# Kernel optimization log

Measured on AMD Instinct MI355X. Metric: run time of the kernel, lower is better.

Reference implementation:

```python
import jax, jax.numpy as jnp
import numpy as np

# dims: batch, history P, horizon Q, hidden D, nodes N, cells C=H*W, Z channels
B_, P_, Q_, D_, N_, C_, H_, W_, CZ = 16, 12, 12, 64, 2000, 1024, 32, 32, 2
K_DIFF = 3  # max diffusion step of DCGRUCell -> K+1 Chebyshev terms


def _mlp2(x, w1, b1, w2, b2):
    return jax.nn.relu(x @ w1 + b1) @ w2 + b2


def _st_embedding(SE, TE, sw1, sb1, sw2, sb2, tw1, tb1, tw2, tb2):
    # GMAN-style spatio-temporal embedding: SE (M,D), TE (B,P,2) ints
    se = _mlp2(SE, sw1, sb1, sw2, sb2)                                  # (M, D)
    te = jnp.concatenate([jax.nn.one_hot(TE[..., 0], 7, dtype=SE.dtype),
                          jax.nn.one_hot(TE[..., 1], 288, dtype=SE.dtype)], axis=-1)
    te = _mlp2(te, tw1, tb1, tw2, tb2)                                  # (B, P, D)
    return se[None, None] + te[:, :, None, :]                           # (B, P, M, D)


def _scaled_laplacian(adj):
    # DCRNN 'laplacian' filter: L_tilde = 2 L / lambda_max - I, lambda_max ~= 2
    A = jnp.maximum(adj, adj.T)
    d = A.sum(axis=1)
    dinv = jnp.where(d > 0, jax.lax.rsqrt(d), 0.0)
    eye = jnp.eye(A.shape[0], dtype=A.dtype)
    L = eye - (dinv[:, None] * A) * dinv[None, :]
    return L - eye


def _gconv(x, L, K):
    # Chebyshev diffusion features: x (B,N,F) -> (B,N,F*(K+1))
    xs = [x, jnp.einsum('nm,bmf->bnf', L, x)]
    for _ in range(2, K + 1):
        xs.append(2.0 * jnp.einsum('nm,bmf->bnf', L, xs[-1]) - xs[-2])
    b, n, f = x.shape
    return jnp.stack(xs, axis=-1).reshape(b, n, f * (K + 1))


def _hard_sigmoid(x):
    return jnp.clip(0.2 * x + 0.5, 0.0, 1.0)


def _conv2d(x, w):
    return jax.lax.conv_general_dilated(x, w, (1, 1), 'SAME',
        dimension_numbers=('NHWC', 'HWIO', 'NHWC'))


def _forward(X, Z, TE, adj_gg, adj_gr, gumbel_noise, se_x, se_z, movement_logits,
             stex_se_w1, stex_se_b1, stex_se_w2, stex_se_b2,
             stex_te_w1, stex_te_b1, stex_te_w2, stex_te_b2,
             stez_se_w1, stez_se_b1, stez_se_w2, stez_se_b2,
             stez_te_w1, stez_te_b1, stez_te_w2, stez_te_b2,
             fcs_z_w1, fcs_z_b1, fcs_z_w2, fcs_z_b2,
             fcs_x_in_w1, fcs_x_in_b1, fcs_x_in_w2, fcs_x_in_b2,
             mov_fc_w, mov_fc_b,
             fcs_x_out_w1, fcs_x_out_b1, fcs_x_out_w2, fcs_x_out_b2,
             convlstm_wx, convlstm_wh,
             dcgru_gate_w, dcgru_gate_b, dcgru_cand_w, dcgru_cand_b):
    B = X.shape[0]
    TEp = TE.astype(jnp.int32)[:, :P_, :]
    # --- cell branch ---
    STEZ = _st_embedding(se_z, TEp, stez_se_w1, stez_se_b1, stez_se_w2, stez_se_b2,
                         stez_te_w1, stez_te_b1, stez_te_w2, stez_te_b2)
    Zf = _mlp2(Z, fcs_z_w1, fcs_z_b1, fcs_z_w2, fcs_z_b2) + STEZ          # (B,P,C,D)
    Zg = Zf.reshape(B, P_, H_, W_, D_)
    def clstm_step(carry, x):
        h, c = carry
        gates = _conv2d(x, convlstm_wx) + _conv2d(h, convlstm_wh)         # (B,H,W,4D)
        i, f, g, o = jnp.split(gates, 4, axis=-1)
        c = _hard_sigmoid(f) * c + _hard_sigmoid(i) * jnp.tanh(g)
        h = _hard_sigmoid(o) * jnp.tanh(c)
        return (h, c), h
    hc0 = (jnp.zeros((B, H_, W_, D_), X.dtype), jnp.zeros((B, H_, W_, D_), X.dtype))
    _, hs = jax.lax.scan(clstm_step, hc0, jnp.swapaxes(Zg, 0, 1))
    Zc = jnp.swapaxes(hs, 0, 1).reshape(B, P_, C_, D_)
    # gumbel-softmax routing over cells (soft, tau=1)
    g = -jnp.log(-jnp.log(gumbel_noise + 1e-20) + 1e-20)
    mZ = jax.nn.softmax(movement_logits + g, axis=-1)                     # (C,C)
    Zc = jnp.einsum('cd,bpdk->bpck', mZ, Zc)
    Zc = jax.nn.relu(Zc @ mov_fc_w + mov_fc_b)
    ZX = jnp.einsum('nc,bpck->bpnk', adj_gr, Zc)                          # (B,P,N,D)
    # --- node branch ---
    STEX = _st_embedding(se_x, TEp, stex_se_w1, stex_se_b1, stex_se_w2, stex_se_b2,
                         stex_te_w1, stex_te_b1, stex_te_w2, stex_te_b2)
    Xf = _mlp2(X[..., None], fcs_x_in_w1, fcs_x_in_b1, fcs_x_in_w2, fcs_x_in_b2) + STEX + ZX
    L = _scaled_laplacian(adj_gg)
    def dcgru_step(h, x):
        xh = jnp.concatenate([x, h], axis=-1)                             # (B,N,2D)
        ru = jax.nn.sigmoid(_gconv(xh, L, K_DIFF) @ dcgru_gate_w + dcgru_gate_b)
        r, u = jnp.split(ru, 2, axis=-1)
        cnd = jnp.tanh(_gconv(jnp.concatenate([x, r * h], axis=-1), L, K_DIFF)
                       @ dcgru_cand_w + dcgru_cand_b)
        return u * h + (1.0 - u) * cnd, None
    h_last, _ = jax.lax.scan(dcgru_step, jnp.zeros((B, N_, D_), X.dtype),
                             jnp.swapaxes(Xf, 0, 1))                      # (B,N,D)
    Y = _mlp2(h_last, fcs_x_out_w1, fcs_x_out_b1, fcs_x_out_w2, fcs_x_out_b2)  # (B,N,Q)
    return jnp.transpose(Y, (0, 2, 1))                                    # (B,Q,N)


def setup_inputs() -> dict:
    key = jax.random.key(0)
    ks = iter(jax.random.split(key, 64))
    def rn(shape, s=0.05):
        return jax.random.normal(next(ks), shape, dtype=jnp.float32) * s
    def ru(shape):
        return jax.random.uniform(next(ks), shape, dtype=jnp.float32)
    z = lambda *s: jnp.zeros(s, jnp.float32)
    NM = K_DIFF + 1
    inp = {
        'X': rn((B_, P_, N_), 1.0),
        'Z': rn((B_, P_, C_, CZ), 1.0),
        'TE': jax.random.randint(next(ks), (B_, P_ + Q_, 2), 0, 7, dtype=jnp.int32),
        'adj_gg': ru((N_, N_)),
        'adj_gr': ru((N_, C_)) * 0.01,
        'gumbel_noise': jnp.clip(ru((C_, C_)), 1e-6, 1.0 - 1e-6),
        'se_x': rn((N_, D_)), 'se_z': rn((C_, D_)),
        'movement_logits': rn((C_, C_)),
        'stex_se_w1': rn((D_, D_)), 'stex_se_b1': z(D_), 'stex_se_w2': rn((D_, D_)), 'stex_se_b2': z(D_),
        'stex_te_w1': rn((295, D_)), 'stex_te_b1': z(D_), 'stex_te_w2': rn((D_, D_)), 'stex_te_b2': z(D_),
        'stez_se_w1': rn((D_, D_)), 'stez_se_b1': z(D_), 'stez_se_w2': rn((D_, D_)), 'stez_se_b2': z(D_),
        'stez_te_w1': rn((295, D_)), 'stez_te_b1': z(D_), 'stez_te_w2': rn((D_, D_)), 'stez_te_b2': z(D_),
        'fcs_z_w1': rn((CZ, D_)), 'fcs_z_b1': z(D_), 'fcs_z_w2': rn((D_, D_)), 'fcs_z_b2': z(D_),
        'fcs_x_in_w1': rn((1, D_)), 'fcs_x_in_b1': z(D_), 'fcs_x_in_w2': rn((D_, D_)), 'fcs_x_in_b2': z(D_),
        'mov_fc_w': rn((D_, D_)), 'mov_fc_b': z(D_),
        'fcs_x_out_w1': rn((D_, D_)), 'fcs_x_out_b1': z(D_), 'fcs_x_out_w2': rn((D_, Q_)), 'fcs_x_out_b2': z(Q_),
        'convlstm_wx': rn((3, 3, D_, 4 * D_)), 'convlstm_wh': rn((3, 3, D_, 4 * D_)),
        'dcgru_gate_w': rn((2 * D_ * NM, 2 * D_)), 'dcgru_gate_b': z(2 * D_),
        'dcgru_cand_w': rn((2 * D_ * NM, D_)), 'dcgru_cand_b': z(D_),
    }
    return inp


def reference(X, Z, TE, adj_gg, adj_gr, gumbel_noise, se_x, se_z, movement_logits,
              stex_se_w1, stex_se_b1, stex_se_w2, stex_se_b2,
              stex_te_w1, stex_te_b1, stex_te_w2, stex_te_b2,
              stez_se_w1, stez_se_b1, stez_se_w2, stez_se_b2,
              stez_te_w1, stez_te_b1, stez_te_w2, stez_te_b2,
              fcs_z_w1, fcs_z_b1, fcs_z_w2, fcs_z_b2,
              fcs_x_in_w1, fcs_x_in_b1, fcs_x_in_w2, fcs_x_in_b2,
              mov_fc_w, mov_fc_b,
              fcs_x_out_w1, fcs_x_out_b1, fcs_x_out_w2, fcs_x_out_b2,
              convlstm_wx, convlstm_wh,
              dcgru_gate_w, dcgru_gate_b, dcgru_cand_w, dcgru_cand_b):
    return _forward(X, Z, TE, adj_gg, adj_gr, gumbel_noise, se_x, se_z, movement_logits,
                    stex_se_w1, stex_se_b1, stex_se_w2, stex_se_b2,
                    stex_te_w1, stex_te_b1, stex_te_w2, stex_te_b2,
                    stez_se_w1, stez_se_b1, stez_se_w2, stez_se_b2,
                    stez_te_w1, stez_te_b1, stez_te_w2, stez_te_b2,
                    fcs_z_w1, fcs_z_b1, fcs_z_w2, fcs_z_b2,
                    fcs_x_in_w1, fcs_x_in_b1, fcs_x_in_w2, fcs_x_in_b2,
                    mov_fc_w, mov_fc_b,
                    fcs_x_out_w1, fcs_x_out_b1, fcs_x_out_w2, fcs_x_out_b2,
                    convlstm_wx, convlstm_wh,
                    dcgru_gate_w, dcgru_gate_b, dcgru_cand_w, dcgru_cand_b)
```

## Files before the change

kernel.cpp:

```cpp
#include <hip/hip_runtime.h>
#include <hip/hip_bf16.h>
#include <math.h>

typedef _Float16 fp16;
typedef _Float16 f16x8 __attribute__((ext_vector_type(8)));
typedef float f32x4 __attribute__((ext_vector_type(4)));

#define BB 16
#define PP 12
#define QQ 12
#define NN 2000
#define CC 1024
#define GP 34
#define GP2 1156

static __device__ __forceinline__ float ldf(float v) { return v; }
static __device__ __forceinline__ float ldf(fp16 v) { return (float)v; }
static __device__ __forceinline__ void stf(float* p, float v) { *p = v; }
static __device__ __forceinline__ void stf(fp16* p, float v) { *p = (fp16)v; }

static __device__ __forceinline__ void gload_lds16(const fp16* g, fp16* l) {
  __builtin_amdgcn_global_load_lds(
      (const __attribute__((address_space(1))) void*)g,
      (__attribute__((address_space(3))) void*)l, 16, 0, 0);
}


__global__ void k_f2h(fp16* __restrict__ dst, const float* __restrict__ src, long long n) {
  long long i = (long long)blockIdx.x * 256 + threadIdx.x;
  if (i < n) dst[i] = (fp16)src[i];
}

__global__ void k_wcatT(fp16* __restrict__ dst, const float* __restrict__ w39,
                        const float* __restrict__ w40) {
  int i = blockIdx.x * 256 + threadIdx.x;
  if (i >= 1152 * 256) return;
  int n = i & 255, kk = i >> 8;
  float v = (kk < 576) ? w39[kk * 256 + n] : w40[(kk - 576) * 256 + n];
  dst[(long long)n * 1152 + kk] = (fp16)v;
}

__global__ void k_gru_repackT(fp16* __restrict__ dst, const float* __restrict__ src, int O) {
  int i = blockIdx.x * 256 + threadIdx.x;
  if (i >= O * 512) return;
  int d = i >> 9;
  int kc = i & 511;
  int t = kc >> 7;
  int c = kc & 127;
  dst[i] = (fp16)src[(c * 4 + t) * O + d];
}

__global__ void k_w2T(fp16* __restrict__ dst, const float* __restrict__ src) {
  int i = blockIdx.x * 256 + threadIdx.x;
  if (i >= 4096) return;
  int d = i >> 6, k = i & 63;
  dst[i] = (fp16)src[k * 64 + d];
}

__global__ void k_wT(fp16* __restrict__ dst, const float* __restrict__ src, int J, int JP) {
  int i = blockIdx.x * 256 + threadIdx.x;
  if (i >= JP * 64) return;
  int j = i >> 6, k = i & 63;
  dst[i] = (fp16)((j < J) ? src[k * J + j] : 0.f);
}

__global__ void k_dinv(const float* __restrict__ adj, float* __restrict__ dinv) {
  int row = blockIdx.x;
  float s = 0.f;
  for (int j = threadIdx.x; j < NN; j += 256)
    s += fmaxf(adj[(long long)row * NN + j], adj[(long long)j * NN + row]);
  __shared__ float red[256];
  red[threadIdx.x] = s;
// ... 11 lines not shown
__global__ void k_L(const float* __restrict__ adj, const float* __restrict__ dinv,
                    fp16* __restrict__ Lh) {
  long long i = (long long)blockIdx.x * 256 + threadIdx.x;
  if (i >= (long long)NN * NN) return;
  int r = (int)(i / NN), c = (int)(i % NN);
  float a = fmaxf(adj[(long long)r * NN + c], adj[(long long)c * NN + r]);
  Lh[(long long)r * 2048 + c] = (fp16)(-dinv[r] * a * dinv[c]);
}

__global__ void k_subdiag(fp16* __restrict__ M2) {
  int i = blockIdx.x * 256 + threadIdx.x;
  if (i >= NN) return;
  M2[(long long)i * 2048 + i] = (fp16)((float)M2[(long long)i * 2048 + i] - 1.0f);
}

__global__ void k_gumbel_softmax(const float* __restrict__ ml, const float* __restrict__ gn,
                                 fp16* __restrict__ mZ) {
  int row = blockIdx.x;
  __shared__ float buf[CC];
  __shared__ float red[256];
  int t = threadIdx.x;
  float mx = -1e30f;
  for (int j = t; j < CC; j += 256) {
    float u = gn[(long long)row * CC + j];
    float g = -logf(-logf(u + 1e-20f) + 1e-20f);
    float v = ml[(long long)row * CC + j] + g;
    buf[j] = v;
    mx = fmaxf(mx, v);
  }
  red[t] = mx;
  __syncthreads();
  for (int st = 128; st > 0; st >>= 1) {
    if (t < st) red[t] = fmaxf(red[t], red[t + st]);
    __syncthreads();
  }
  mx = red[0];
  __syncthreads();
  float s = 0.f;
  for (int j = t; j < CC; j += 256) {
    float e = expf(buf[j] - mx);
    buf[j] = e;
    s += e;
  }
  red[t] = s;
  __syncthreads();
  for (int st = 128; st > 0; st >>= 1) {
    if (t < st) red[t] += red[t + st];
    __syncthreads();
  }
  float inv = 1.0f / red[0];
  for (int j = t; j < CC; j += 256) mZ[(long long)row * CC + j] = (fp16)(buf[j] * inv);
}

__global__ void k_te(const int* __restrict__ TE, const float* __restrict__ w1,
                     const float* __restrict__ b1, float* __restrict__ tmp) {
  int i = blockIdx.x * 256 + threadIdx.x;
  if (i >= BB * PP * 64) return;
  int j = i & 63;
  int bp = i >> 6;
  int b = bp / PP, p = bp % PP;
  int te0 = TE[(b * (PP + QQ) + p) * 2 + 0];
  int te1 = TE[(b * (PP + QQ) + p) * 2 + 1];
  float v = w1[te0 * 64 + j] + w1[(7 + te1) * 64 + j] + b1[j];
  tmp[i] = fmaxf(v, 0.f);
}

__global__ void k_addb(float* __restrict__ dst, const float* __restrict__ b, int n) {
  int i = blockIdx.x * 256 + threadIdx.x;
  if (i < n) dst[i] += b[i & 63];
}

__global__ __launch_bounds__(256) void k_zf2f(
    const float* __restrict__ Z, const float* __restrict__ w25,
    const float* __restrict__ b26, const fp16* __restrict__ w27T,
    const float* __restrict__ b28, const float* __restrict__ seZ,
    const float* __restrict__ teZ, fp16* __restrict__ Zfp) {
  __shared__ fp16 As[128 * 64];
  __shared__ fp16 Bs[64 * 64];
  const int tid = threadIdx.x;
  const int gm0 = blockIdx.x * 128;
  const int lane = tid & 63, wv = tid >> 6;
  const int wr = wv >> 1, wc = wv & 1;
  const int quad = lane >> 4, ln = lane & 15;
#pragma unroll
  for (int i = 0; i < 4; ++i) {
    int c = i * 256 + tid;
    int row = c >> 3, seg = c & 7;
    float z0v = Z[(long long)(gm0 + row) * 2 + 0];
    float z1v = Z[(long long)(gm0 + row) * 2 + 1];
    fp16 tmp[8];
#pragma unroll
    for (int e = 0; e < 8; ++e) {
      int j = seg * 8 + e;
      tmp[e] = (fp16)fmaxf(z0v * w25[j] + z1v * w25[64 + j] + b26[j], 0.f);
    }
    *(f16x8*)&As[row * 64 + ((seg ^ (row & 7)) * 8)] = *(f16x8*)tmp;
  }
#pragma unroll
  for (int i = 0; i < 2; ++i) {
    int c = i * 256 + tid;
    int row = c >> 3;
    int lseg = (c & 7) ^ (row & 7);
    gload_lds16(w27T + (long long)row * 64 + lseg * 8, &Bs[c * 8]);
  }
  f32x4 acc[4][2];
#pragma unroll
  for (int i = 0; i < 4; ++i)
#pragma unroll
    for (int j = 0; j < 2; ++j) acc[i][j] = (f32x4){0.f, 0.f, 0.f, 0.f};
  __syncthreads();
#pragma unroll
  for (int kt = 0; kt < 2; ++kt) {
    f16x8 af[4], bf[2];
#pragma unroll
    for (int wm = 0; wm < 4; ++wm) {
      int row = wr * 64 + wm * 16 + ln;
      int slot = (kt * 4 + quad) ^ (row & 7);
      af[wm] = *(const f16x8*)&As[row * 64 + slot * 8];
    }
#pragma unroll
    for (int wn = 0; wn < 2; ++wn) {
      int row = wc * 32 + wn * 16 + ln;
// ... 63 lines not shown
    f16x8 af[4], bf[2];
#pragma unroll
    for (int wm = 0; wm < 4; ++wm) {
      int row = wr * 64 + wm * 16 + ln;
      af[wm] = *(const f16x8*)&hT[row * 72 + kt * 32 + quad * 8];
    }
#pragma unroll
    for (int wn = 0; wn < 2; ++wn) {
      int row = wc * 32 + wn * 16 + ln;
      int slot = (kt * 4 + quad) ^ (row & 7);
      bf[wn] = *(const f16x8*)&Bs[row * 64 + slot * 8];
    }
#pragma unroll
    for (int wm = 0; wm < 4; ++wm)
#pragma unroll
      for (int wn = 0; wn < 2; ++wn)
        a1[wm][wn] =
            __builtin_amdgcn_mfma_f32_16x16x32_f16(af[wm], bf[wn], a1[wm][wn], 0, 0, 0);
  }
#pragma unroll
  for (int wm = 0; wm < 4; ++wm)
#pragma unroll
    for (int wn = 0; wn < 2; ++wn)
#pragma unroll
      for (int r = 0; r < 4; ++r) {
        int rl = wr * 64 + wm * 16 + quad * 4 + r;
        int j = wc * 32 + wn * 16 + ln;
        h2[rl * 72 + j] = (fp16)fmaxf(a1[wm][wn][r] + b36[j], 0.f);
      }
  __syncthreads();
  f32x4 a2[2];
#pragma unroll
  for (int i = 0; i < 2; ++i) a2[i] = (f32x4){0.f, 0.f, 0.f, 0.f};
#pragma unroll
  for (int kt = 0; kt < 2; ++kt) {
    f16x8 bf = *(const f16x8*)(w37T + ln * 64 + kt * 32 + quad * 8);
#pragma unroll
    for (int wm = 0; wm < 2; ++wm) {
      int row = wv * 32 + wm * 16 + ln;
      f16x8 af = *(const f16x8*)&h2[row * 72 + kt * 32 + quad * 8];
      a2[wm] = __builtin_amdgcn_mfma_f32_16x16x32_f16(af, bf, a2[wm], 0, 0, 0);
    }
  }
#pragma unroll
  for (int wm = 0; wm < 2; ++wm)
#pragma unroll
    for (int r = 0; r < 4; ++r) {
      int nl = wv * 32 + wm * 16 + quad * 4 + r;
      int n = n0 + nl;
      int q = ln;
      if (n < NN && q < 12)
        out[((long long)b * 12 + q) * NN + n] = a2[wm][r] + b38[q];
    }
}

template <typename TA, typename TB, typename TC>
__global__ __launch_bounds__(256) void gemm_t(
    const TA* __restrict__ A, int lda, long long sA,
    const TB* __restrict__ Bm, int ldb, long long sB,
    TC* Cm, int ldc, long long sC,
    const TC* S, long long sS,
    const float* __restrict__ bias,
    int M, int Ncols, int K, float alpha, float beta, int act) {
  int bz = blockIdx.z;
  A += (long long)bz * sA;
  Bm += (long long)bz * sB;
  Cm += (long long)bz * sC;
  if (S) S += (long long)bz * sS;
  const int row0 = blockIdx.x * 64, col0 = blockIdx.y * 64;
  __shared__ float As[16][68];
  __shared__ float Bs[16][68];
  int tid = threadIdx.x, tx = tid & 15, ty = tid >> 4;
  float acc[4][4] = {};
  for (int k0 = 0; k0 < K; k0 += 16) {
#pragma unroll
    for (int j = 0; j < 4; ++j) {
      int e = tid + 256 * j;
      int m = e >> 4, kk = e & 15;
      int gm = row0 + m;
      As[kk][m] = (gm < M) ? ldf(A[(long long)gm * lda + k0 + kk]) : 0.f;
    }
#pragma unroll
    for (int j = 0; j < 4; ++j) {
      int e = tid + 256 * j;
      int kk = e >> 6, n = e & 63;
      int gn = col0 + n;
      Bs[kk][n] = (gn < Ncols) ? ldf(Bm[(long long)(k0 + kk) * ldb + gn]) : 0.f;
    }
    __syncthreads();
#pragma unroll
    for (int kk = 0; kk < 16; ++kk) {
      float a[4], bb[4];
#pragma unroll
      for (int i = 0; i < 4; ++i) a[i] = As[kk][ty * 4 + i];
#pragma unroll
      for (int j = 0; j < 4; ++j) bb[j] = Bs[kk][tx * 4 + j];
#pragma unroll
      for (int i = 0; i < 4; ++i)
#pragma unroll
        for (int j = 0; j < 4; ++j) acc[i][j] = fmaf(a[i], bb[j], acc[i][j]);
    }
    __syncthreads();
  }
#pragma unroll
  for (int i = 0; i < 4; ++i) {
    int r = row0 + ty * 4 + i;
    if (r >= M) continue;
#pragma unroll
    for (int j = 0; j < 4; ++j) {
      int cn = col0 + tx * 4 + j;
      if (cn >= Ncols) continue;
      float v = alpha * acc[i][j];
      if (bias) v += bias[cn];
      if (S) v += beta * ldf(S[(long long)r * ldc + cn]);
      if (act == 1) v = fmaxf(v, 0.f);
      else if (act == 2) v = 1.f / (1.f + expf(-v));
      else if (act == 3) v = tanhf(v);
      stf(&Cm[(long long)r * ldc + cn], v);
    }
  }
}

template <int MT, int MODE>
__global__ __launch_bounds__(256) void mfma7(
    const fp16* __restrict__ A,
    const fp16* __restrict__ U0base, long long uZ, int bHi,
    const fp16* __restrict__ xB, long long xZ,
    const fp16* __restrict__ Xc, long long XcSlab, int Xcld, int Xczmul,
    const fp16* __restrict__ Hc, long long HcSlab, int Hcld, int Hczmul,
    fp16* __restrict__ C, int ldc, long long cBatch,
    const float* __restrict__ bias,
    fp16* __restrict__ rhOut, const fp16* __restrict__ hIn,
    const fp16* __restrict__ uIn, long long uStride,
    int M, int Ncols) {
  __shared__ fp16 As[2][MT * 32];
  __shared__ fp16 Bs[2][64 * 32];
  const int z = blockIdx.z;
  const int n0 = blockIdx.y * 64;
  const fp16* U0z = U0base + (long long)z * uZ;
  const fp16* xBz = xB + (long long)z * xZ;
  C += (long long)z * cBatch;
  if (rhOut) rhOut += (long long)z * uZ;
  if (hIn) hIn += (long long)z * uZ;
  if (uIn) uIn += (long long)z * uStride;
  const int tid = threadIdx.x;
  const int lane = tid & 63, wv = tid >> 6;
  const int wr = wv >> 1, wc = wv & 1;
  const int quad = lane >> 4, ln = lane & 15;
  constexpr int WM = MT / 32;

  const fp16* aSrc[MT / 64];
#pragma unroll
  for (int i = 0; i < MT / 64; ++i) {
    int c = i * 256 + tid;
    int row = c >> 2;
    int lseg = (c & 3) ^ ((c >> 3) & 3);
    aSrc[i] = A + (long long)row * 512 + lseg * 8;
  }
  const int brow = tid >> 2;
  const int blseg = (tid & 3) ^ ((tid >> 3) & 3);
  const long long bnode = n0 + brow;

  f32x4 acc[WM][2];
#pragma unroll
  for (int i = 0; i < WM; ++i)
#pragma unroll
    for (int j = 0; j < 2; ++j) acc[i][j] = (f32x4){0.f, 0.f, 0.f, 0.f};

  auto stage = [&](int t, int buf) {
    const int k0 = t * 32;
#pragma unroll
    for (int i = 0; i < MT / 64; ++i)
      gload_lds16(aSrc[i] + k0, &As[buf][(i * 256 + tid) * 8]);
// ... 337 lines not shown

  const int sw = (quad ^ ((ln >> 1) & 3)) << 3;

#pragma unroll
  for (int i = 0; i < MT / 64; ++i) gload_lds16(aSrc[i], &As[0][(i * 256 + tid) * 8]);
#pragma unroll
  for (int i = 0; i < NT / 64; ++i) gload_lds16(bSrc[i], &Bs[0][(i * 256 + tid) * 8]);

  const int nk = K >> 5;
  for (int t = 0; t < nk; ++t) {
    const int buf = t & 1;
    __syncthreads();
    if (t + 1 < nk) {
      const int k1 = (t + 1) * 32;
#pragma unroll
      for (int i = 0; i < MT / 64; ++i)
        gload_lds16(aSrc[i] + k1, &As[buf ^ 1][(i * 256 + tid) * 8]);
#pragma unroll
      for (int i = 0; i < NT / 64; ++i)
        gload_lds16(bSrc[i] + k1, &Bs[buf ^ 1][(i * 256 + tid) * 8]);
    }
    f16x8 af[WM], bf[WN];
#pragma unroll
    for (int wm = 0; wm < WM; ++wm) {
      int row = wr * (MT / 2) + wm * 16 + ln;
      af[wm] = *(const f16x8*)&As[buf][row * 32 + sw];
    }
#pragma unroll
    for (int wn = 0; wn < WN; ++wn) {
      int row = wc * (NT / 2) + wn * 16 + ln;
      bf[wn] = *(const f16x8*)&Bs[buf][row * 32 + sw];
    }
#pragma unroll
    for (int wm = 0; wm < WM; ++wm)
#pragma unroll
      for (int wn = 0; wn < WN; ++wn)
        acc[wm][wn] =
            __builtin_amdgcn_mfma_f32_16x16x32_f16(af[wm], bf[wn], acc[wm][wn], 0, 0, 0);
  }
#pragma unroll
  for (int wm = 0; wm < WM; ++wm)
#pragma unroll
    for (int wn = 0; wn < WN; ++wn)
#pragma unroll
      for (int r = 0; r < 4; ++r) {
        int gm = gm0 + wr * (MT / 2) + wm * 16 + quad * 4 + r;
        int gn = n0 + wc * (NT / 2) + wn * 16 + ln;
        long long ci = ((long long)((unsigned)gm >> cMsh)) * cMslab +
                       (long long)(gm & cMmask) * ldc + gn;
        C[ci] = (fp16)acc[wm][wn][r];
      }
}

__global__ __launch_bounds__(256) void k_zxtfin2(
    const fp16* __restrict__ w2T, const float* __restrict__ X,
    const float* __restrict__ w29, const float* __restrict__ b30,
    fp16* __restrict__ ZXt, const float* __restrict__ teXb,
    const float* __restrict__ seX) {
  __shared__ fp16 As[64][72];
  __shared__ fp16 Bs[128][72];
  const int z = blockIdx.z;
  const int n0 = blockIdx.y * 128;
  fp16* Cz = ZXt + (long long)z * 64 * 2048;
  const float* tb = teXb + z * 64;
  const int tid = threadIdx.x;
  const int lane = tid & 63, wv = tid >> 6;
  const int wr = wv >> 1, wc = wv & 1;
  const int quad = lane >> 4, ln = lane & 15;
#pragma unroll
  for (int i = 0; i < 2; ++i) {
    int c = tid + 256 * i;
    int row = c >> 3, seg = c & 7;
    *(f16x8*)&As[row][seg * 8] = *(const f16x8*)(w2T + row * 64 + seg * 8);
  }
#pragma unroll
  for (int i = 0; i < 4; ++i) {
    int c = tid + 256 * i;
    int row = c >> 3, seg = c & 7;
    int n = n0 + row;
    float xv = (n < NN) ? X[(long long)z * NN + n] : 0.f;
    fp16 tmp[8];
#pragma unroll
    for (int e = 0; e < 8; ++e) {
      int j = seg * 8 + e;
      tmp[e] = (fp16)fmaxf(xv * w29[j] + b30[j], 0.f);
    }
    *(f16x8*)&Bs[row][seg * 8] = *(f16x8*)tmp;
  }
  __syncthreads();
  f32x4 acc[2][4];
#pragma unroll
  for (int i = 0; i < 2; ++i)
#pragma unroll
    for (int j = 0; j < 4; ++j) acc[i][j] = (f32x4){0.f, 0.f, 0.f, 0.f};
#pragma unroll
  for (int kt = 0; kt < 2; ++kt) {
    f16x8 af[2], bf[4];
#pragma unroll
    for (int wm = 0; wm < 2; ++wm)
      af[wm] = *(const f16x8*)&As[wr * 32 + wm * 16 + ln][kt * 32 + quad * 8];
#pragma unroll
    for (int wn = 0; wn < 4; ++wn)
      bf[wn] = *(const f16x8*)&Bs[wc * 64 + wn * 16 + ln][kt * 32 + quad * 8];
#pragma unroll
    for (int wm = 0; wm < 2; ++wm)
#pragma unroll
      for (int wn = 0; wn < 4; ++wn)
        acc[wm][wn] =
            __builtin_amdgcn_mfma_f32_16x16x32_f16(af[wm], bf[wn], acc[wm][wn], 0, 0, 0);
  }
#pragma unroll
  for (int wm = 0; wm < 2; ++wm)
#pragma unroll
    for (int wn = 0; wn < 4; ++wn)
#pragma unroll
      for (int r = 0; r < 4; ++r) {
        int gm = wr * 32 + wm * 16 + quad * 4 + r;
        int gn = n0 + wc * 64 + wn * 16 + ln;
        long long ci = (long long)gm * 2048 + gn;
        float v = 0.f;
        if (gn < NN)
          v = acc[wm][wn][r] + (float)Cz[ci] + tb[gm] + seX[(long long)gn * 64 + gm];
        Cz[ci] = (fp16)v;
      }
}

__global__ __launch_bounds__(256) void k_conv4(
    const fp16* __restrict__ Zfp, const fp16* __restrict__ hp,
    const fp16* __restrict__ wcatT, fp16* __restrict__ gates, int p) {
  __shared__ fp16 As[2][128 * 32];
  __shared__ fp16 Bs[2][64 * 32];
  const int gm0 = blockIdx.x * 128, n0 = blockIdx.y * 64;
  const int tid = threadIdx.x;
  const int lane = tid & 63, wv = tid >> 6;
  const int wr = wv >> 1, wc = wv & 1;
  const int quad = lane >> 4, ln = lane & 15;

  long long aZ[2], aH[2];
#pragma unroll
  for (int i = 0; i < 2; ++i) {
    int c = tid + 256 * i;
    int row = c >> 2;
    int lseg = (c & 3) ^ ((c >> 3) & 3);
    int m = gm0 + row;
    int b = m >> 10, y = (m >> 5) & 31, x = m & 31;
    int pc = (y + 1) * GP + (x + 1);
    aZ[i] = ((long long)(b * PP + p) * GP2 + pc) * 64 + lseg * 8;
    aH[i] = ((long long)b * GP2 + pc) * 64 + lseg * 8;
  }
  const fp16* bBase;
  {
    int row = tid >> 2;
    int lseg = (tid & 3) ^ ((tid >> 3) & 3);
    bBase = wcatT + (long long)(n0 + row) * 1152 + lseg * 8;
  }
  f32x4 acc[4][2];
#pragma unroll
  for (int i = 0; i < 4; ++i)
#pragma unroll
    for (int j = 0; j < 2; ++j) acc[i][j] = (f32x4){0.f, 0.f, 0.f, 0.f};

  auto stage = [&](int t, int buf) {
    int tap = (t >> 1) % 9, half = t & 1;
    int srcsel = t >= 18;
    int off = ((tap / 3 - 1) * GP + (tap % 3 - 1)) * 64 + half * 32;
#pragma unroll
    for (int i = 0; i < 2; ++i) {
      const fp16* src = srcsel ? (hp + aH[i] + off) : (Zfp + aZ[i] + off);
      gload_lds16(src, &As[buf][(i * 256 + tid) * 8]);
    }
    gload_lds16(bBase + t * 32, &Bs[buf][tid * 8]);
  };
  stage(0, 0);
  const int sw = (quad ^ ((ln >> 1) & 3)) << 3;
  for (int t = 0; t < 36; ++t) {
    const int buf = t & 1;
// ... 1 lines not shown
    if (t + 1 < 36) stage(t + 1, buf ^ 1);
    f16x8 af[4], bf[2];
#pragma unroll
    for (int wm = 0; wm < 4; ++wm) {
      int row = wr * 64 + wm * 16 + ln;
      af[wm] = *(const f16x8*)&As[buf][row * 32 + sw];
    }
#pragma unroll
    for (int wn = 0; wn < 2; ++wn) {
      int row = wc * 32 + wn * 16 + ln;
      bf[wn] = *(const f16x8*)&Bs[buf][row * 32 + sw];
    }
#pragma unroll
    for (int wm = 0; wm < 4; ++wm)
#pragma unroll
      for (int wn = 0; wn < 2; ++wn)
        acc[wm][wn] =
            __builtin_amdgcn_mfma_f32_16x16x32_f16(af[wm], bf[wn], acc[wm][wn], 0, 0, 0);
  }
#pragma unroll
  for (int wm = 0; wm < 4; ++wm)
#pragma unroll
    for (int wn = 0; wn < 2; ++wn)
#pragma unroll
      for (int r = 0; r < 4; ++r) {
        int gm = gm0 + wr * 64 + wm * 16 + quad * 4 + r;
        int gn = n0 + wc * 32 + wn * 16 + ln;
        gates[(long long)gm * 256 + gn] = (fp16)acc[wm][wn][r];
      }
}

__global__ void k_clstm_update(const fp16* __restrict__ gates, float* __restrict__ c,
                               fp16* __restrict__ h, fp16* __restrict__ ZclT, int p) {
  long long i = (long long)blockIdx.x * 256 + threadIdx.x;
  if (i >= (long long)BB * CC * 64) return;
  int d = (int)(i & 63);
  long long bc = i >> 6;
  int b = (int)(bc >> 10);
  int cell = (int)(bc & 1023);
  const fp16* g = gates + (((long long)b * CC) + cell) * 256;
  float gi = (float)g[d], gf = (float)g[64 + d], gg = (float)g[128 + d],
        go = (float)g[192 + d];
  float hs_f = fminf(fmaxf(0.2f * gf + 0.5f, 0.f), 1.f);
  float hs_i = fminf(fmaxf(0.2f * gi + 0.5f, 0.f), 1.f);
  float hs_o = fminf(fmaxf(0.2f * go + 0.5f, 0.f), 1.f);
  float cv = hs_f * c[i] + hs_i * tanhf(gg);
  c[i] = cv;
  float hv = hs_o * tanhf(cv);
  int pc = ((cell >> 5) + 1) * GP + (cell & 31) + 1;
  h[((long long)b * GP2 + pc) * 64 + d] = (fp16)hv;
  ZclT[(((long long)(b * PP + p)) * 64 + d) * CC + cell] = (fp16)hv;
}

template <typename TA, typename TB, typename TC>
static void launch_gemm(hipStream_t stream, const TA* A, int lda, long long sA,
                        const TB* Bm, int ldb, long long sB, TC* Cm, int ldc, long long sC,
                        const TC* S, long long sS, const float* bias, int M, int Nc, int K,
                        float alpha, float beta, int act, int batch) {
  dim3 g((M + 63) / 64, (Nc + 63) / 64, batch);
  gemm_t<TA, TB, TC><<<g, dim3(256), 0, stream>>>(A, lda, sA, Bm, ldb, sB, Cm, ldc, sC, S,
                                                  sS, bias, M, Nc, K, alpha, beta, act);
}

extern "C" void kernel_launch(void* const* d_in, const int* in_sizes, int n_in,
                              void* d_out, int out_size, void* d_ws, size_t ws_size,
                              hipStream_t stream) {
  char* base = (char*)d_ws;
  size_t off = 0;
  auto alloc_bytes = [&](size_t nb) -> char* {
    char* p = base + off;
    off += (nb + 255) & ~(size_t)255;
    return p;
  };
  auto allocf = [&](size_t n) -> float* { return (float*)alloc_bytes(n * 4); };
  auto alloch = [&](size_t n) -> fp16* { return (fp16*)alloc_bytes(n * 2); };

  const float* X = (const float*)d_in[0];
  const float* Z = (const float*)d_in[1];
  const int* TE = (const int*)d_in[2];
  const float* adj_gg = (const float*)d_in[3];
  const float* adj_gr = (const float*)d_in[4];
  const float* gumbel = (const float*)d_in[5];
  const float* se_x = (const float*)d_in[6];
  const float* se_z = (const float*)d_in[7];
  const float* movement = (const float*)d_in[8];
  auto W = [&](int i) { return (const float*)d_in[i]; };

  fp16* wcatT = alloch((size_t)256 * 1152);
  fp16* gwT = alloch(128 * 512);
  fp16* cwT = alloch(64 * 512);
  fp16* w2T = alloch(64 * 64);
  fp16* w2mT = alloch(64 * 64);
  fp16* w27T = alloch(64 * 64);
  fp16* w35T = alloch(64 * 64);
  fp16* w37T = alloch(16 * 64);
  float* dinv = allocf(NN);
  fp16* LMall = alloch((size_t)6144 * 2048);
  fp16* mZh = alloch((size_t)CC * CC);
  fp16* agh2 = alloch((size_t)2048 * CC);
  float* seZ = allocf(CC * 64);
  float* teZ = allocf(BB * PP * 64);
  float* seX = allocf(NN * 64);
  float* teXb = allocf(BB * PP * 64);
  float* mtmp = allocf(NN * 64);
  float* tetmp = allocf(BB * PP * 64);
  fp16* ruT = alloch((size_t)BB * 128 * NN);
  char* pool = alloc_bytes(50331648);
  fp16* Uall = (fp16*)pool;
  fp16* gates = (fp16*)pool;
  fp16* chh = (fp16*)(pool + 8388608);
  float* ccc = (float*)(pool + 12582912);
  fp16* Zmix = (fp16*)pool;
  fp16* ZmovT = (fp16*)(pool + 25165824);
  fp16* zpool = alloch((size_t)BB * PP * 64 * 2048);
  fp16* Zfp = zpool;
  fp16* ZXt = zpool;
  fp16* Zc = alloch((size_t)BB * PP * CC * 64);

  if (off > ws_size) return;

  const long long uB = 192LL * 2048;
  const long long USL = 16LL * uB;
  const long long ZXB = 12LL * 64 * 2048;
  fp16* Lh = LMall;
  fp16* M2h = LMall + 2048LL * 2048;
  fp16* M3h = LMall + 4096LL * 2048;
  const int KCH = 2016;

  k_wcatT<<<dim3(1152), dim3(256), 0, stream>>>(wcatT, W(39), W(40));
  k_gru_repackT<<<dim3(256), dim3(256), 0, stream>>>(gwT, W(41), 128);
  k_gru_repackT<<<dim3(128), dim3(256), 0, stream>>>(cwT, W(43), 64);
  k_w2T<<<dim3(16), dim3(256), 0, stream>>>(w2T, W(31));
  k_w2T<<<dim3(16), dim3(256), 0, stream>>>(w2mT, W(33));
  k_wT<<<dim3(16), dim3(256), 0, stream>>>(w27T, W(27), 64, 64);
  k_wT<<<dim3(16), dim3(256), 0, stream>>>(w35T, W(35), 64, 64);
  k_wT<<<dim3(4), dim3(256), 0, stream>>>(w37T, W(37), 12, 16);
  k_dinv<<<dim3(NN), dim3(256), 0, stream>>>(adj_gg, dinv);
  hipMemsetAsync(LMall, 0, (size_t)6144 * 2048 * 2, stream);
  k_L<<<dim3((NN * NN + 255) / 256), dim3(256), 0, stream>>>(adj_gg, dinv, Lh);
  mfma4<64, 128><<<dim3(32, 16, 1), dim3(256), 0, stream>>>(
      Lh, Lh, 31, 31, 0LL, 0LL, 2048, Lh, 2048, 0LL, M2h, 2048, 0LL, 31, 0LL, 31, 0LL,
      (const fp16*)nullptr, 2.f, 0.f, KCH);
  k_subdiag<<<dim3((NN + 255) / 256), dim3(256), 0, stream>>>(M2h);
  mfma4<64, 128><<<dim3(32, 16, 1), dim3(256), 0, stream>>>(
      Lh, Lh, 31, 31, 0LL, 0LL, 2048, M2h, 2048, 0LL, M3h, 2048, 0LL, 31, 0LL, 31, 0LL,
      (const fp16*)Lh, 2.f, -1.f, KCH);
  k_gumbel_softmax<<<dim3(CC), dim3(256), 0, stream>>>(movement, gumbel, mZh);
  k_f2h<<<dim3((NN * CC + 255) / 256), dim3(256), 0, stream>>>(agh2, adj_gr,
                                                               (long long)NN * CC);
  hipMemsetAsync(agh2 + (size_t)NN * CC, 0, (size_t)(2048 - NN) * CC * 2, stream);

  launch_gemm(stream, se_z, 64, 0LL, W(17), 64, 0LL, mtmp, 64, 0LL, (float*)nullptr, 0LL,
              W(18), CC, 64, 64, 1.f, 0.f, 1, 1);
  launch_gemm(stream, (const float*)mtmp, 64, 0LL, W(19), 64, 0LL, seZ, 64, 0LL,
              (float*)nullptr, 0LL, W(20), CC, 64, 64, 1.f, 0.f, 0, 1);
  k_te<<<dim3((BB * PP * 64 + 255) / 256), dim3(256), 0, stream>>>(TE, W(21), W(22), tetmp);
  launch_gemm(stream, (const float*)tetmp, 64, 0LL, W(23), 64, 0LL, teZ, 64, 0LL,
              (float*)nullptr, 0LL, W(24), BB * PP, 64, 64, 1.f, 0.f, 0, 1);
  launch_gemm(stream, se_x, 64, 0LL, W(9), 64, 0LL, mtmp, 64, 0LL, (float*)nullptr, 0LL,
              W(10), NN, 64, 64, 1.f, 0.f, 1, 1);
  launch_gemm(stream, (const float*)mtmp, 64, 0LL, W(11), 64, 0LL, seX, 64, 0LL,
              (float*)nullptr, 0LL, W(12), NN, 64, 64, 1.f, 0.f, 0, 1);
  k_te<<<dim3((BB * PP * 64 + 255) / 256), dim3(256), 0, stream>>>(TE, W(13), W(14), tetmp);
  launch_gemm(stream, (const float*)tetmp, 64, 0LL, W(15), 64, 0LL, teXb, 64, 0LL,
              (float*)nullptr, 0LL, W(16), BB * PP, 64, 64, 1.f, 0.f, 0, 1);
  k_addb<<<dim3((BB * PP * 64 + 255) / 256), dim3(256), 0, stream>>>(teXb, W(32),
                                                                     BB * PP * 64);

  hipMemsetAsync(zpool, 0, (size_t)BB * PP * GP2 * 64 * 2, stream);
  k_zf2f<<<dim3(1536), dim3(256), 0, stream>>>(Z, W(25), W(26), w27T, W(28), seZ, teZ,
                                               Zfp);

  hipMemsetAsync(chh, 0, (size_t)BB * GP2 * 64 * 2, stream);
  hipMemsetAsync(ccc, 0, (size_t)BB * CC * 64 * 4, stream);
  for (int p = 0; p < PP; ++p) {
    k_conv4<<<dim3(BB * CC / 128, 4), dim3(256), 0, stream>>>(Zfp, chh, wcatT, gates, p);
    k_clstm_update<<<dim3((int)(((long long)BB * CC * 64 + 255) / 256)), dim3(256), 0,
                     stream>>>(gates, ccc, chh, Zc, p);
  }

  mfma4<128, 64><<<dim3(8, 1, 192), dim3(256), 0, stream>>>(
      mZh, mZh, 31, 31, 0LL, 0LL, CC, (const fp16*)Zc, CC, (long long)64 * CC, Zmix, 64,
      (long long)CC * 64, 31, 0LL, 31, 0LL, (const fp16*)nullptr, 1.f, 0.f, CC);
  mfma3<64, 128><<<dim3(1, 8, 192), dim3(256), 0, stream>>>(
      w2mT, 64, 0LL, 31, 0LL, Zmix, 64, (long long)CC * 64, ZmovT, CC, (long long)64 * CC,
      31, 0LL, 31, 0LL, (const fp16*)nullptr, 0LL, 0.f, W(34), 0LL, nullptr, 0, 64, CC, 64,
      1.f, 1);

  mfma4<128, 128><<<dim3(96, 16, 1), dim3(256), 0, stream>>>(
      ZmovT, ZmovT, 31, 31, 0LL, 0LL, 1024, agh2, 1024, 0LL, ZXt, 2048, 0LL, 31, 0LL, 31,
      0LL, (const fp16*)nullptr, 1.f, 0.f, 1024);

  k_zxtfin2<<<dim3(1, 16, 192), dim3(256), 0, stream>>>(w2T, X, W(29), W(30), ZXt, teXb,
                                                        seX);

  fp16* U0 = Uall;
  fp16* Tn = Uall + USL;
  fp16* Tn2 = Uall + 3 * USL;
  const long long TnSlab = 2048LL * 2048;
  const long long Tn2Slab = 2048LL * 1024;
  hipMemsetAsync(U0, 0, (size_t)USL * 2, stream);

  for (int p = 0; p < PP; ++p) {
    const fp16* xP = ZXt + (long long)p * 64 * 2048;
    mfma6<128, 128><<<dim3(48, 16), dim3(256), 0, stream>>>(
        LMall, 2048, xP, U0 + 64 * 2048, 7, 6, ZXB, uB, 2048, Tn, 2048, 11, TnSlab, KCH);
    mfma7<128, 1><<<dim3(1, 32, BB), dim3(256), 0, stream>>>(
        gwT, U0, uB, 0, xP, ZXB,
        Tn, TnSlab, 2048, 128,
        Tn + 64, TnSlab, 2048, 128,
        ruT, NN, (long long)128 * NN, W(42), U0 + 128 * 2048, U0 + 64 * 2048,
        (const fp16*)nullptr, 0LL, 128, NN);
    mfma6<64, 128><<<dim3(96, 8), dim3(256), 0, stream>>>(
        LMall, 2048, U0 + 128 * 2048, U0 + 128 * 2048, 6, 6, uB, uB, 2048, Tn2, 1024, 11,
        Tn2Slab, KCH);
    mfma7<64, 2><<<dim3(1, 32, BB), dim3(256), 0, stream>>>(
        cwT, U0, uB, 64, xP, ZXB,
        Tn, TnSlab, 2048, 128,
        Tn2, Tn2Slab, 1024, 64,
        U0 + 64 * 2048, 2048, uB, W(44), (fp16*)nullptr, (const fp16*)nullptr,
        (const fp16*)ruT, (long long)128 * NN, 64, NN);
  }

  k_head<<<dim3(16, 16), dim3(256), 0, stream>>>(U0, w35T, W(36), w37T, W(38),
                                                 (float*)d_out);
}
```

Measured before the change: 2.866 ms.

## Fuse embedding MLPs into MFMA kernels and reorder ZXt finalize before GEMM

Replaces the scalar fp32 tiled gemm_t chain (two GEMMs plus k_te and k_addb per embedding) with a single fused two-layer MFMA MLP kernel per embedding. The spatial embedding for X is now written transposed in fp16. The ZXt finalize kernel now runs before the big mfma4 GEMM and writes the bias, embedding and X projection into ZXt. The GEMM then accumulates onto it with beta=1, so the extra read-modify-write pass is dropped. This cuts launch count and small-GEMM overhead, at the cost of fp16 precision in the embedding MLPs.

```diff
diff --git a/kernel.cpp b/kernel.cpp
--- a/kernel.cpp
+++ b/kernel.cpp
@@ -13,11 +13,6 @@
 #define CC 1024
 #define GP 34
 #define GP2 1156
-
-static __device__ __forceinline__ float ldf(float v) { return v; }
-static __device__ __forceinline__ float ldf(fp16 v) { return (float)v; }
-static __device__ __forceinline__ void stf(float* p, float v) { *p = v; }
-static __device__ __forceinline__ void stf(fp16* p, float v) { *p = (fp16)v; }
 
 static __device__ __forceinline__ void gload_lds16(const fp16* g, fp16* l) {
   __builtin_amdgcn_global_load_lds(
@@ -135,22 +130,149 @@
   for (int j = t; j < CC; j += 256) mZ[(long long)row * CC + j] = (fp16)(buf[j] * inv);
 }
 
-__global__ void k_te(const int* __restrict__ TE, const float* __restrict__ w1,
-                     const float* __restrict__ b1, float* __restrict__ tmp) {
-  int i = blockIdx.x * 256 + threadIdx.x;
-  if (i >= BB * PP * 64) return;
-  int j = i & 63;
-  int bp = i >> 6;
-  int b = bp / PP, p = bp % PP;
-  int te0 = TE[(b * (PP + QQ) + p) * 2 + 0];
-  int te1 = TE[(b * (PP + QQ) + p) * 2 + 1];
-  float v = w1[te0 * 64 + j] + w1[(7 + te1) * 64 + j] + b1[j];
-  tmp[i] = fmaxf(v, 0.f);
-}
-
-__global__ void k_addb(float* __restrict__ dst, const float* __restrict__ b, int n) {
-  int i = blockIdx.x * 256 + threadIdx.x;
-  if (i < n) dst[i] += b[i & 63];
+template <int MODE>
+__global__ __launch_bounds__(256) void k_mlp2(
+    const float* __restrict__ A, const int* __restrict__ TE,
+    const float* __restrict__ w1f, const float* __restrict__ b1,
+    const fp16* __restrict__ w1T, const fp16* __restrict__ w2T,
+    const float* __restrict__ b2, const float* __restrict__ eb,
+    float* __restrict__ out, fp16* __restrict__ outT, int M) {
+  __shared__ fp16 hT[128 * 72];
+  __shared__ fp16 Bs[64 * 64];
+  __shared__ fp16 h2[128 * 72];
+  const int m0 = blockIdx.x * 128;
+  const int tid = threadIdx.x;
+  const int lane = tid & 63, wv = tid >> 6;
+  const int wr = wv >> 1, wc = wv & 1;
+  const int quad = lane >> 4, ln = lane & 15;
+#pragma unroll
+  for (int i = 0; i < 4; ++i) {
+    int c = i * 256 + tid;
+    int row = c >> 3, seg = c & 7;
+    int gm = m0 + row;
+    fp16 tmp[8];
+    if (MODE == 0) {
+#pragma unroll
+      for (int e = 0; e < 8; ++e)
+        tmp[e] = (gm < M) ? (fp16)A[(long long)gm * 64 + seg * 8 + e] : (fp16)0.f;
+      *(f16x8*)&hT[row * 72 + seg * 8] = *(f16x8*)tmp;
+    } else {
+      if (gm < M) {
+        int b = gm / PP, p = gm - b * PP;
+        int te0 = TE[(b * (PP + QQ) + p) * 2 + 0];
+        int te1 = TE[(b * (PP + QQ) + p) * 2 + 1];
+#pragma unroll
+        for (int e = 0; e < 8; ++e) {
+          int j = seg * 8 + e;
+          tmp[e] =
+              (fp16)fmaxf(w1f[te0 * 64 + j] + w1f[(7 + te1) * 64 + j] + b1[j], 0.f);
+        }
+      } else {
+#pragma unroll
+        for (int e = 0; e < 8; ++e) tmp[e] = (fp16)0.f;
+      }
+      *(f16x8*)&h2[row * 72 + seg * 8] = *(f16x8*)tmp;
+    }
+  }
+  {
+    const fp16* wsrc = (MODE == 0) ? w1T : w2T;
+#pragma unroll
+    for (int i = 0; i < 2; ++i) {
+      int c = i * 256 + tid;
+      int row = c >> 3, s = c & 7;
+      *(f16x8*)&Bs[row * 64 + ((s ^ (row & 7)) * 8)] =
+          *(const f16x8*)(wsrc + row * 64 + s * 8);
+    }
+  }
+  __syncthreads();
+  if (MODE == 0) {
+    f32x4 a1[4][2];
+#pragma unroll
+    for (int i = 0; i < 4; ++i)
+#pragma unroll
+      for (int j = 0; j < 2; ++j) a1[i][j] = (f32x4){0.f, 0.f, 0.f, 0.f};
+#pragma unroll
+    for (int kt = 0; kt < 2; ++kt) {
+      f16x8 af[4], bf[2];
+#pragma unroll
+      for (int wm = 0; wm < 4; ++wm) {
+        int row = wr * 64 + wm * 16 + ln;
+        af[wm] = *(const f16x8*)&hT[row * 72 + kt * 32 + quad * 8];
+      }
+#pragma unroll
+      for (int wn = 0; wn < 2; ++wn) {
+        int row = wc * 32 + wn * 16 + ln;
+        int slot = (kt * 4 + quad) ^ (row & 7);
+        bf[wn] = *(const f16x8*)&Bs[row * 64 + slot * 8];
+      }
+#pragma unroll
+      for (int wm = 0; wm < 4; ++wm)
+#pragma unroll
+        for (int wn = 0; wn < 2; ++wn)
+          a1[wm][wn] =
+              __builtin_amdgcn_mfma_f32_16x16x32_f16(af[wm], bf[wn], a1[wm][wn], 0, 0, 0);
+    }
+    __syncthreads();
+#pragma unroll
+    for (int wm = 0; wm < 4; ++wm)
+#pragma unroll
+      for (int wn = 0; wn < 2; ++wn)
+#pragma unroll
+        for (int r = 0; r < 4; ++r) {
+          int rl = wr * 64 + wm * 16 + quad * 4 + r;
+          int j = wc * 32 + wn * 16 + ln;
+          h2[rl * 72 + j] = (fp16)fmaxf(a1[wm][wn][r] + b1[j], 0.f);
+        }
+#pragma unroll
+    for (int i = 0; i < 2; ++i) {
+      int c = i * 256 + tid;
+      int row = c >> 3, s = c & 7;
+      *(f16x8*)&Bs[row * 64 + ((s ^ (row & 7)) * 8)] =
+          *(const f16x8*)(w2T + row * 64 + s * 8);
+    }
+    __syncthreads();
+  }
+  f32x4 a2[4][2];
+#pragma unroll
+  for (int i = 0; i < 4; ++i)
+#pragma unroll
+    for (int j = 0; j < 2; ++j) a2[i][j] = (f32x4){0.f, 0.f, 0.f, 0.f};
+#pragma unroll
+  for (int kt = 0; kt < 2; ++kt) {
+    f16x8 af[4], bf[2];
+#pragma unroll
+    for (int wm = 0; wm < 4; ++wm) {
+      int row = wr * 64 + wm * 16 + ln;
+      af[wm] = *(const f16x8*)&h2[row * 72 + kt * 32 + quad * 8];
+    }
+#pragma unroll
+    for (int wn = 0; wn < 2; ++wn) {
+      int row = wc * 32 + wn * 16 + ln;
+      int slot = (kt * 4 + quad) ^ (row & 7);
+      bf[wn] = *(const f16x8*)&Bs[row * 64 + slot * 8];
+    }
+#pragma unroll
+    for (int wm = 0; wm < 4; ++wm)
+#pragma unroll
+      for (int wn = 0; wn < 2; ++wn)
+        a2[wm][wn] =
+            __builtin_amdgcn_mfma_f32_16x16x32_f16(af[wm], bf[wn], a2[wm][wn], 0, 0, 0);
+  }
+#pragma unroll
+  for (int wm = 0; wm < 4; ++wm)
+#pragma unroll
+    for (int wn = 0; wn < 2; ++wn)
+#pragma unroll
+      for (int r = 0; r < 4; ++r) {
+        int gm = m0 + wr * 64 + wm * 16 + quad * 4 + r;
+        int j = wc * 32 + wn * 16 + ln;
+        if (gm < M) {
+          float v = a2[wm][wn][r] + b2[j];
+          if (eb) v += eb[j];
+          if (out) out[(long long)gm * 64 + j] = v;
+          if (outT) outT[(long long)j * 2048 + gm] = (fp16)v;
+        }
+      }
 }
 
 __global__ __launch_bounds__(256) void k_zf2f(
@@ -320,73 +442,6 @@
       if (n < NN && q < 12)
         out[((long long)b * 12 + q) * NN + n] = a2[wm][r] + b38[q];
     }
-}
-
-template <typename TA, typename TB, typename TC>
-__global__ __launch_bounds__(256) void gemm_t(
-    const TA* __restrict__ A, int lda, long long sA,
-    const TB* __restrict__ Bm, int ldb, long long sB,
-    TC* Cm, int ldc, long long sC,
-    const TC* S, long long sS,
-    const float* __restrict__ bias,
-    int M, int Ncols, int K, float alpha, float beta, int act) {
-  int bz = blockIdx.z;
-  A += (long long)bz * sA;
-  Bm += (long long)bz * sB;
-  Cm += (long long)bz * sC;
-  if (S) S += (long long)bz * sS;
-  const int row0 = blockIdx.x * 64, col0 = blockIdx.y * 64;
-  __shared__ float As[16][68];
-  __shared__ float Bs[16][68];
-  int tid = threadIdx.x, tx = tid & 15, ty = tid >> 4;
-  float acc[4][4] = {};
-  for (int k0 = 0; k0 < K; k0 += 16) {
-#pragma unroll
-    for (int j = 0; j < 4; ++j) {
-      int e = tid + 256 * j;
-      int m = e >> 4, kk = e & 15;
-      int gm = row0 + m;
-      As[kk][m] = (gm < M) ? ldf(A[(long long)gm * lda + k0 + kk]) : 0.f;
-    }
-#pragma unroll
-    for (int j = 0; j < 4; ++j) {
-      int e = tid + 256 * j;
-      int kk = e >> 6, n = e & 63;
-      int gn = col0 + n;
-      Bs[kk][n] = (gn < Ncols) ? ldf(Bm[(long long)(k0 + kk) * ldb + gn]) : 0.f;
-    }
-    __syncthreads();
-#pragma unroll
-    for (int kk = 0; kk < 16; ++kk) {
-      float a[4], bb[4];
-#pragma unroll
-      for (int i = 0; i < 4; ++i) a[i] = As[kk][ty * 4 + i];
-#pragma unroll
-      for (int j = 0; j < 4; ++j) bb[j] = Bs[kk][tx * 4 + j];
-#pragma unroll
-      for (int i = 0; i < 4; ++i)
-#pragma unroll
-        for (int j = 0; j < 4; ++j) acc[i][j] = fmaf(a[i], bb[j], acc[i][j]);
-    }
-    __syncthreads();
-  }
-#pragma unroll
-  for (int i = 0; i < 4; ++i) {
-    int r = row0 + ty * 4 + i;
-    if (r >= M) continue;
-#pragma unroll
-    for (int j = 0; j < 4; ++j) {
-      int cn = col0 + tx * 4 + j;
-      if (cn >= Ncols) continue;
-      float v = alpha * acc[i][j];
-      if (bias) v += bias[cn];
-      if (S) v += beta * ldf(S[(long long)r * ldc + cn]);
-      if (act == 1) v = fmaxf(v, 0.f);
-      else if (act == 2) v = 1.f / (1.f + expf(-v));
-      else if (act == 3) v = tanhf(v);
-      stf(&Cm[(long long)r * ldc + cn], v);
-    }
-  }
 }
 
 template <int MT, int MODE>
@@ -830,11 +885,11 @@
       }
 }
 
-__global__ __launch_bounds__(256) void k_zxtfin2(
+__global__ __launch_bounds__(256) void k_zxtfin2w(
     const fp16* __restrict__ w2T, const float* __restrict__ X,
     const float* __restrict__ w29, const float* __restrict__ b30,
     fp16* __restrict__ ZXt, const float* __restrict__ teXb,
-    const float* __restrict__ seX) {
+    const fp16* __restrict__ seXT) {
   __shared__ fp16 As[64][72];
   __shared__ fp16 Bs[128][72];
   const int z = blockIdx.z;
@@ -895,11 +950,10 @@
       for (int r = 0; r < 4; ++r) {
         int gm = wr * 32 + wm * 16 + quad * 4 + r;
         int gn = n0 + wc * 64 + wn * 16 + ln;
-        long long ci = (long long)gm * 2048 + gn;
         float v = 0.f;
         if (gn < NN)
-          v = acc[wm][wn][r] + (float)Cz[ci] + tb[gm] + seX[(long long)gn * 64 + gm];
-        Cz[ci] = (fp16)v;
+          v = acc[wm][wn][r] + tb[gm] + (float)seXT[(long long)gm * 2048 + gn];
+        Cz[(long long)gm * 2048 + gn] = (fp16)v;
       }
 }
 
@@ -1007,16 +1061,6 @@
   ZclT[(((long long)(b * PP + p)) * 64 + d) * CC + cell] = (fp16)hv;
 }
 
-template <typename TA, typename TB, typename TC>
-static void launch_gemm(hipStream_t stream, const TA* A, int lda, long long sA,
-                        const TB* Bm, int ldb, long long sB, TC* Cm, int ldc, long long sC,
-                        const TC* S, long long sS, const float* bias, int M, int Nc, int K,
-                        float alpha, float beta, int act, int batch) {
-  dim3 g((M + 63) / 64, (Nc + 63) / 64, batch);
-  gemm_t<TA, TB, TC><<<g, dim3(256), 0, stream>>>(A, lda, sA, Bm, ldb, sB, Cm, ldc, sC, S,
-                                                  sS, bias, M, Nc, K, alpha, beta, act);
-}
-
 extern "C" void kernel_launch(void* const* d_in, const int* in_sizes, int n_in,
                               void* d_out, int out_size, void* d_ws, size_t ws_size,
                               hipStream_t stream) {
@@ -1049,16 +1093,20 @@
   fp16* w27T = alloch(64 * 64);
   fp16* w35T = alloch(64 * 64);
   fp16* w37T = alloch(16 * 64);
+  fp16* w9T = alloch(64 * 64);
+  fp16* w11T = alloch(64 * 64);
+  fp16* w17T = alloch(64 * 64);
+  fp16* w19T = alloch(64 * 64);
+  fp16* w15T = alloch(64 * 64);
+  fp16* w23T = alloch(64 * 64);
   float* dinv = allocf(NN);
   fp16* LMall = alloch((size_t)6144 * 2048);
   fp16* mZh = alloch((size_t)CC * CC);
   fp16* agh2 = alloch((size_t)2048 * CC);
   float* seZ = allocf(CC * 64);
   float* teZ = allocf(BB * PP * 64);
-  float* seX = allocf(NN * 64);
+  fp16* seXT = alloch((size_t)64 * 2048);
   float* teXb = allocf(BB * PP * 64);
-  float* mtmp = allocf(NN * 64);
-  float* tetmp = allocf(BB * PP * 64);
   fp16* ruT = alloch((size_t)BB * 128 * NN);
   char* pool = alloc_bytes(50331648);
   fp16* Uall = (fp16*)pool;
@@ -1090,6 +1138,12 @@
   k_wT<<<dim3(16), dim3(256), 0, stream>>>(w27T, W(27), 64, 64);
   k_wT<<<dim3(16), dim3(256), 0, stream>>>(w35T, W(35), 64, 64);
   k_wT<<<dim3(4), dim3(256), 0, stream>>>(w37T, W(37), 12, 16);
+  k_wT<<<dim3(16), dim3(256), 0, stream>>>(w9T, W(9), 64, 64);
+  k_wT<<<dim3(16), dim3(256), 0, stream>>>(w11T, W(11), 64, 64);
+  k_wT<<<dim3(16), dim3(256), 0, stream>>>(w17T, W(17), 64, 64);
+  k_wT<<<dim3(16), dim3(256), 0, stream>>>(w19T, W(19), 64, 64);
+  k_wT<<<dim3(16), dim3(256), 0, stream>>>(w15T, W(15), 64, 64);
+  k_wT<<<dim3(16), dim3(256), 0, stream>>>(w23T, W(23), 64, 64);
   k_dinv<<<dim3(NN), dim3(256), 0, stream>>>(adj_gg, dinv);
   hipMemsetAsync(LMall, 0, (size_t)6144 * 2048 * 2, stream);
   k_L<<<dim3((NN * NN + 255) / 256), dim3(256), 0, stream>>>(adj_gg, dinv, Lh);
@@ -1105,22 +1159,21 @@
                                                                (long long)NN * CC);
   hipMemsetAsync(agh2 + (size_t)NN * CC, 0, (size_t)(2048 - NN) * CC * 2, stream);
 
-  launch_gemm(stream, se_z, 64, 0LL, W(17), 64, 0LL, mtmp, 64, 0LL, (float*)nullptr, 0LL,
-              W(18), CC, 64, 64, 1.f, 0.f, 1, 1);
-  launch_gemm(stream, (const float*)mtmp, 64, 0LL, W(19), 64, 0LL, seZ, 64, 0LL,
-              (float*)nullptr, 0LL, W(20), CC, 64, 64, 1.f, 0.f, 0, 1);
-  k_te<<<dim3((BB * PP * 64 + 255) / 256), dim3(256), 0, stream>>>(TE, W(21), W(22), tetmp);
-  launch_gemm(stream, (const float*)tetmp, 64, 0LL, W(23), 64, 0LL, teZ, 64, 0LL,
-              (float*)nullptr, 0LL, W(24), BB * PP, 64, 64, 1.f, 0.f, 0, 1);
-  launch_gemm(stream, se_x, 64, 0LL, W(9), 64, 0LL, mtmp, 64, 0LL, (float*)nullptr, 0LL,
-              W(10), NN, 64, 64, 1.f, 0.f, 1, 1);
-  launch_gemm(stream, (const float*)mtmp, 64, 0LL, W(11), 64, 0LL, seX, 64, 0LL,
-              (float*)nullptr, 0LL, W(12), NN, 64, 64, 1.f, 0.f, 0, 1);
-  k_te<<<dim3((BB * PP * 64 + 255) / 256), dim3(256), 0, stream>>>(TE, W(13), W(14), tetmp);
-  launch_gemm(stream, (const float*)tetmp, 64, 0LL, W(15), 64, 0LL, teXb, 64, 0LL,
-              (float*)nullptr, 0LL, W(16), BB * PP, 64, 64, 1.f, 0.f, 0, 1);
-  k_addb<<<dim3((BB * PP * 64 + 255) / 256), dim3(256), 0, stream>>>(teXb, W(32),
-                                                                     BB * PP * 64);
+  k_mlp2<0><<<dim3(8), dim3(256), 0, stream>>>(se_z, (const int*)nullptr,
+                                               (const float*)nullptr, W(18), w17T, w19T,
+                                               W(20), (const float*)nullptr, seZ,
+                                               (fp16*)nullptr, CC);
+  k_mlp2<0><<<dim3(16), dim3(256), 0, stream>>>(se_x, (const int*)nullptr,
+                                                (const float*)nullptr, W(10), w9T, w11T,
+                                                W(12), (const float*)nullptr,
+                                                (float*)nullptr, seXT, NN);
+  k_mlp2<1><<<dim3(2), dim3(256), 0, stream>>>((const float*)nullptr, TE, W(21), W(22),
+                                               (const fp16*)nullptr, w23T, W(24),
+                                               (const float*)nullptr, teZ, (fp16*)nullptr,
+                                               BB * PP);
+  k_mlp2<1><<<dim3(2), dim3(256), 0, stream>>>((const float*)nullptr, TE, W(13), W(14),
+                                               (const fp16*)nullptr, w15T, W(16), W(32),
+                                               teXb, (fp16*)nullptr, BB * PP);
 
   hipMemsetAsync(zpool, 0, (size_t)BB * PP * GP2 * 64 * 2, stream);
   k_zf2f<<<dim3(1536), dim3(256), 0, stream>>>(Z, W(25), W(26), w27T, W(28), seZ, teZ,
@@ -1142,12 +1195,12 @@
       31, 0LL, 31, 0LL, (const fp16*)nullptr, 0LL, 0.f, W(34), 0LL, nullptr, 0, 64, CC, 64,
       1.f, 1);
 
+  k_zxtfin2w<<<dim3(1, 16, 192), dim3(256), 0, stream>>>(w2T, X, W(29), W(30), ZXt, teXb,
+                                                         seXT);
+
   mfma4<128, 128><<<dim3(96, 16, 1), dim3(256), 0, stream>>>(
       ZmovT, ZmovT, 31, 31, 0LL, 0LL, 1024, agh2, 1024, 0LL, ZXt, 2048, 0LL, 31, 0LL, 31,
-      0LL, (const fp16*)nullptr, 1.f, 0.f, 1024);
-
-  k_zxtfin2<<<dim3(1, 16, 192), dim3(256), 0, stream>>>(w2T, X, W(29), W(30), ZXt, teXb,
-                                                        seX);
+      0LL, (const fp16*)ZXt, 1.f, 1.f, 1024);
 
   fp16* U0 = Uall;
   fp16* Tn = Uall + USL;
```

Result: faster. 2.784 ms (-2.9%).
